# Performance work log

Hardware: AMD Instinct MI355X
Metric: run time of the kernel (lower is better)

Reference implementation:

```python
import jax, jax.numpy as jnp
import numpy as np

B, S, D, H, HD, FF, W = 2, 4096, 2048, 16, 128, 8192, 256
EPS = 1e-6
ROPE_BASE = 10000.0


def rmsnorm(x, w):
    return x * jax.lax.rsqrt(jnp.mean(x * x, axis=-1, keepdims=True) + EPS) * w


def apply_rope(x):
    # x: [B, H, S, hd]
    hd = x.shape[-1]
    inv = 1.0 / (ROPE_BASE ** (jnp.arange(0, hd, 2, dtype=jnp.float32) / hd))
    ang = jnp.arange(x.shape[2], dtype=jnp.float32)[:, None] * inv[None, :]  # [S, hd/2]
    cos, sin = jnp.cos(ang), jnp.sin(ang)
    x1, x2 = jnp.split(x, 2, axis=-1)
    return jnp.concatenate([x1 * cos - x2 * sin, x1 * sin + x2 * cos], axis=-1)


def setup_inputs() -> dict:
    key = jax.random.key(0)
    ks = jax.random.split(key, 12)
    sc = 0.02
    return {
        "x": jax.random.normal(ks[0], (B, S, D), jnp.float32),
        "Wq": jax.random.normal(ks[1], (D, D), jnp.float32) * sc,
        "Wk": jax.random.normal(ks[2], (D, D), jnp.float32) * sc,
        "Wv": jax.random.normal(ks[3], (D, D), jnp.float32) * sc,
        "Wo": jax.random.normal(ks[4], (D, D), jnp.float32) * sc,
        "qn_w": jnp.ones((HD,), jnp.float32),
        "kn_w": jnp.ones((HD,), jnp.float32),
        "sink_logit": jax.random.normal(ks[5], (H,), jnp.float32) * sc,
        "attn_norm_w": jnp.ones((D,), jnp.float32),
        "ffn_norm_w": jnp.ones((D,), jnp.float32),
        "Wg": jax.random.normal(ks[6], (D, FF), jnp.float32) * sc,
        "Wu": jax.random.normal(ks[7], (D, FF), jnp.float32) * sc,
        "Wd": jax.random.normal(ks[8], (FF, D), jnp.float32) * sc,
    }


def reference(x, Wq, Wk, Wv, Wo, qn_w, kn_w, sink_logit, attn_norm_w, ffn_norm_w, Wg, Wu, Wd):
    # ---- sliding-window attention sublayer ----
    h = rmsnorm(x, attn_norm_w)
    q = (h @ Wq).reshape(B, S, H, HD)
    k = (h @ Wk).reshape(B, S, H, HD)
    v = (h @ Wv).reshape(B, S, H, HD)
    q = rmsnorm(q, qn_w)
    k = rmsnorm(k, kn_w)
    q = apply_rope(q.transpose(0, 2, 1, 3))  # [B,H,S,hd]
    k = apply_rope(k.transpose(0, 2, 1, 3))
    v = v.transpose(0, 2, 1, 3)

    nb = S // W
    qb = q.reshape(B, H, nb, W, HD)
    kb = k.reshape(B, H, nb, W, HD)
    vb = v.reshape(B, H, nb, W, HD)
    # each query block attends to previous block + own block (window=W causal)
    kprev = jnp.concatenate([jnp.zeros_like(kb[:, :, :1]), kb[:, :, :-1]], axis=2)
    vprev = jnp.concatenate([jnp.zeros_like(vb[:, :, :1]), vb[:, :, :-1]], axis=2)
    kl = jnp.concatenate([kprev, kb], axis=3)  # [B,H,nb,2W,hd]
    vl = jnp.concatenate([vprev, vb], axis=3)

    qi = jnp.arange(W)
    kj = jnp.arange(2 * W)
    rel = W + qi[:, None] - kj[None, :]  # q_pos - kv_pos within block pair
    base = (rel >= 0) & (rel < W)  # causal + in-window, [W, 2W]
    blk = jnp.arange(nb)
    kv_pos_valid = (blk[:, None, None] * W - W + kj[None, None, :]) >= 0  # [nb,1,2W]
    mask = base[None, :, :] & kv_pos_valid  # [nb, W, 2W]

    scale = 1.0 / jnp.sqrt(jnp.float32(HD))
    scores = jnp.einsum("bhnqd,bhnkd->bhnqk", qb, kl) * scale
    scores = jnp.where(mask[None, None], scores, jnp.float32(-1e30))
    # attention sink: virtual kv slot 0 with per-head logit, zero value
    sink = jnp.broadcast_to(sink_logit.reshape(1, H, 1, 1, 1), scores.shape[:-1] + (1,))
    logits = jnp.concatenate([sink, scores], axis=-1)
    p = jax.nn.softmax(logits, axis=-1)
    out = jnp.einsum("bhnqk,bhnkd->bhnqd", p[..., 1:], vl)  # sink contributes 0
    out = out.reshape(B, H, S, HD).transpose(0, 2, 1, 3).reshape(B, S, D)
    x = x + out @ Wo

    # ---- SwiGLU FFN sublayer ----
    h2 = rmsnorm(x, ffn_norm_w)
    x = x + (jax.nn.silu(h2 @ Wg) * (h2 @ Wu)) @ Wd
    return x
```

## Files before the change

### kernel.cpp

```cpp
#include <hip/hip_runtime.h>
#include <hip/hip_bf16.h>
#include <stdint.h>

typedef __bf16 bf16_t;
typedef __bf16 bf16x8 __attribute__((ext_vector_type(8)));
typedef float f32x4 __attribute__((ext_vector_type(4)));

#define B_ 2
#define S_ 4096
#define D_ 2048
#define H_ 16
#define HD_ 128
#define FF_ 8192
#define W_ 256
#define NB_ 16
#define ROWS_ 8192
#define QS_ 6144

#define BAR() asm volatile("s_barrier" ::: "memory")

__device__ __forceinline__ bool det_bf16(const uint32_t* det) {
  return (det[0] & 0xFFFFu) == 0x3F80u;
}
__device__ __forceinline__ float ldS(const void* p, size_t i, bool isbf) {
  return isbf ? (float)((const bf16_t*)p)[i] : ((const float*)p)[i];
}
__device__ __forceinline__ void ld8(const void* p, size_t i, bool isbf,
                                    float* f) {
  if (isbf) {
    bf16x8 v = *(const bf16x8*)((const bf16_t*)p + i);
#pragma unroll
    for (int j = 0; j < 8; ++j) f[j] = (float)v[j];
  } else {
    const float* s = (const float*)p + i;
    float4 a = *(const float4*)s;
    float4 b = *(const float4*)(s + 4);
    f[0] = a.x; f[1] = a.y; f[2] = a.z; f[3] = a.w;
    f[4] = b.x; f[5] = b.y; f[6] = b.z; f[7] = b.w;
  }
}

__device__ __forceinline__ void gld_lds16(const bf16_t* g, bf16_t* l) {
  __builtin_amdgcn_global_load_lds(
      (const __attribute__((address_space(1))) uint32_t*)g,
      (__attribute__((address_space(3))) uint32_t*)l, 16, 0, 0);
}

__global__ __launch_bounds__(256)
void transpose_k(const void* __restrict__ src, bf16_t* __restrict__ dst,
                 int R, int C, const uint32_t* __restrict__ det) {
  __shared__ __align__(16) bf16_t tile[64][72];
  const bool isbf = det_bf16(det);
  const int nbc = C >> 6;
  const int br = blockIdx.x / nbc, bc = blockIdx.x % nbc;
  const int t = threadIdx.x;
#pragma unroll
  for (int rnd = 0; rnd < 2; ++rnd) {
    int chunk = t + rnd * 256;
    int r = chunk >> 3;
    int c8 = (chunk & 7) << 3;
    float f[8];
    ld8(src, (size_t)(br * 64 + r) * C + bc * 64 + c8, isbf, f);
    union { bf16_t e[8]; int4 v; } u;
#pragma unroll
    for (int j = 0; j < 8; ++j) u.e[j] = (bf16_t)f[j];
    *(int4*)&tile[r][c8] = u.v;
  }
  __syncthreads();
#pragma unroll
  for (int rnd = 0; rnd < 2; ++rnd) {
    int chunk = t + rnd * 256;
    int cc = chunk >> 3;
    int r8 = (chunk & 7) << 3;
    union { bf16_t e[8]; int4 v; } u;
#pragma unroll
    for (int j = 0; j < 8; ++j) u.e[j] = tile[r8 + j][cc];
    *(int4*)&dst[(size_t)(bc * 64 + cc) * R + br * 64 + r8] = u.v;
  }
}

__global__ __launch_bounds__(256)
void rmsnorm_in_k(const void* __restrict__ x, const void* __restrict__ w,
                  bf16_t* __restrict__ out, const uint32_t* __restrict__ det) {
  __shared__ float sm[4];
  const bool isbf = det_bf16(det);
  const size_t row = blockIdx.x;
  const int i0 = threadIdx.x << 3;
  float f[8], ss = 0.f;
  ld8(x, row * D_ + i0, isbf, f);
#pragma unroll
  for (int j = 0; j < 8; ++j) ss += f[j] * f[j];
#pragma unroll
  for (int off = 1; off < 64; off <<= 1) ss += __shfl_xor(ss, off, 64);
  if ((threadIdx.x & 63) == 0) sm[threadIdx.x >> 6] = ss;
  __syncthreads();
  float tot = sm[0] + sm[1] + sm[2] + sm[3];
  float rs = rsqrtf(tot * (1.0f / D_) + 1e-6f);
  float wf[8];
  ld8(w, i0, isbf, wf);
  bf16x8 res;
#pragma unroll
  for (int j = 0; j < 8; ++j) res[j] = (bf16_t)(f[j] * rs * wf[j]);
  *(bf16x8*)&out[row * D_ + i0] = res;
}

__global__ __launch_bounds__(256)
void rmsnorm_f32_k(const float* __restrict__ x, const void* __restrict__ w,
                   bf16_t* __restrict__ out, const uint32_t* __restrict__ det) {
  __shared__ float sm[4];
  const bool isbf = det_bf16(det);
  const size_t row = blockIdx.x;
  const int i0 = threadIdx.x << 3;
  float4 a = *(const float4*)&x[row * D_ + i0];
  float4 b = *(const float4*)&x[row * D_ + i0 + 4];
  float f[8] = {a.x, a.y, a.z, a.w, b.x, b.y, b.z, b.w};
  float ss = 0.f;
#pragma unroll
  for (int j = 0; j < 8; ++j) ss += f[j] * f[j];
#pragma unroll
  for (int off = 1; off < 64; off <<= 1) ss += __shfl_xor(ss, off, 64);
  if ((threadIdx.x & 63) == 0) sm[threadIdx.x >> 6] = ss;
  __syncthreads();
  float tot = sm[0] + sm[1] + sm[2] + sm[3];
  float rs = rsqrtf(tot * (1.0f / D_) + 1e-6f);
  float wf[8];
  ld8(w, i0, isbf, wf);
  bf16x8 res;
#pragma unroll
  for (int j = 0; j < 8; ++j) res[j] = (bf16_t)(f[j] * rs * wf[j]);
  *(bf16x8*)&out[row * D_ + i0] = res;
}

__global__ __launch_bounds__(256)
void qknorm_rope_k(bf16_t* __restrict__ qkv, const void* __restrict__ qw,
                   const void* __restrict__ kw,
                   const uint32_t* __restrict__ det) {
  const bool isbf = det_bf16(det);
  const int wv = threadIdx.x >> 6;
  const int i = threadIdx.x & 63;
  const int idx = blockIdx.x * 4 + wv;
  const int row = idx >> 4;
  const int s = row & (S_ - 1);
  const int h = idx & 15;
  bf16_t* qp = qkv + (size_t)row * QS_ + h * HD_;
  bf16_t* kp = qp + 2048;

  float inv = exp2f((float)i * -0.20762050593046014f);
  float ang = (float)s * inv;
  float sn, cs;
  sincosf(ang, &sn, &cs);

#pragma unroll
  for (int t = 0; t < 2; ++t) {
    bf16_t* p = (t == 0) ? qp : kp;
    const void* w = (t == 0) ? qw : kw;
    float x1 = (float)p[i], x2 = (float)p[i + 64];
    float ss = x1 * x1 + x2 * x2;
#pragma unroll
    for (int off = 1; off < 64; off <<= 1) ss += __shfl_xor(ss, off, 64);
    float rs = rsqrtf(ss * (1.0f / HD_) + 1e-6f);
    float n1 = x1 * rs * ldS(w, i, isbf);
    float n2 = x2 * rs * ldS(w, i + 64, isbf);
    p[i] = (bf16_t)(n1 * cs - n2 * sn);
    p[i + 64] = (bf16_t)(n1 * sn + n2 * cs);
  }
}

#define TQ 8192

template <int EPI>
__global__ __launch_bounds__(512, 2)
void gemm256_k(const bf16_t* __restrict__ A, const bf16_t* __restrict__ Bt,
               void* __restrict__ C, const void* __restrict__ aux,
               const uint32_t* __restrict__ det, int M, int N, int K) {
  extern __shared__ __align__(16) bf16_t lds[];
  bf16_t* Ab = lds;
  bf16_t* Bb = lds + 2 * TQ;

  bool isbf = false;
  if constexpr (EPI == 1 || EPI == 3) isbf = det_bf16(det);

  const int tid = threadIdx.x;
  const int lane = tid & 63, wid = tid >> 6;
  const int l15 = lane & 15, l4 = lane >> 4;
  const int wm = wid >> 2, wn = wid & 3;

  const int nwg = gridDim.x;
  const int nbn = N >> 8;
  const int orig = blockIdx.x;
  const int q8 = nwg >> 3, r8 = nwg & 7, xcd = orig & 7;
  const int swz = (xcd < r8 ? xcd * (q8 + 1) : r8 * (q8 + 1) + (xcd - r8) * q8)
                + (orig >> 3);
  const int grp = swz / (4 * nbn);
  const int rem = swz % (4 * nbn);
  const int bm = grp * 4 + (rem & 3);
  const int bn = rem >> 2;

  const bf16_t* Ag = A + (size_t)(bm * 256) * K;
  const bf16_t* Bg = Bt + (size_t)(bn * 256) * K;

  const int c0 = tid, c1 = 512 + tid;
  const int r0 = c0 >> 2, r1 = c1 >> 2;
  const size_t goff0 = (size_t)r0 * K + (((c0 & 3) ^ ((r0 >> 1) & 3)) << 3);
  const size_t goff1 = (size_t)r1 * K + (((c1 & 3) ^ ((r1 >> 1) & 3)) << 3);
  const int loff0 = c0 * 8, loff1 = c1 * 8;

  auto stage = [&](int tt) {
    bf16_t* la = Ab + (tt & 1) * TQ;
    bf16_t* lb = Bb + (tt & 1) * TQ;
    const size_t k0 = (size_t)tt << 5;
    gld_lds16(Ag + k0 + goff0, la + loff0);
    gld_lds16(Ag + k0 + goff1, la + loff1);
    gld_lds16(Bg + k0 + goff0, lb + loff0);
    gld_lds16(Bg + k0 + goff1, lb + loff1);
  };

  int aoff[8], boff[4];
#pragma unroll
  for (int m = 0; m < 8; ++m) {
    int R = wm * 128 + m * 16 + l15;
    aoff[m] = R * 32 + ((l4 ^ ((R >> 1) & 3)) << 3);
  }
#pragma unroll
  for (int n = 0; n < 4; ++n) {
    int R = wn * 64 + n * 16 + l15;
    boff[n] = R * 32 + ((l4 ^ ((R >> 1) & 3)) << 3);
  }

  f32x4 acc[8][4] = {};
  const int nt = K >> 5;

  stage(0);
  asm volatile("s_waitcnt vmcnt(0)" ::: "memory");
  BAR();

  for (int t = 0; t < nt; ++t) {
    const bf16_t* a = Ab + (t & 1) * TQ;
    const bf16_t* b = Bb + (t & 1) * TQ;

    if (t + 1 < nt) stage(t + 1);

    bf16x8 af[8], bfr[4];
#pragma unroll
    for (int n = 0; n < 4; ++n) bfr[n] = *(const bf16x8*)&b[boff[n]];
#pragma unroll
    for (int m = 0; m < 8; ++m) af[m] = *(const bf16x8*)&a[aoff[m]];

#pragma unroll
    for (int m = 0; m < 8; ++m)
#pragma unroll
      for (int n = 0; n < 4; ++n)
        acc[m][n] = __builtin_amdgcn_mfma_f32_16x16x32_bf16(af[m], bfr[n],
                                                            acc[m][n], 0, 0, 0);

    asm volatile("s_waitcnt vmcnt(0)" ::: "memory");
    BAR();
  }

#pragma unroll
  for (int m8 = 0; m8 < 8; ++m8) {
#pragma unroll
    for (int r = 0; r < 4; ++r) {
      const int row = bm * 256 + wm * 128 + m8 * 16 + l4 * 4 + r;
#pragma unroll
      for (int n = 0; n < 4; ++n) {
        const int col = bn * 256 + wn * 64 + n * 16 + l15;
        const size_t idx = (size_t)row * N + col;
        const float val = acc[m8][n][r];
        if constexpr (EPI == 0) {
          ((bf16_t*)C)[idx] = (bf16_t)val;
        } else if constexpr (EPI == 1) {
          ((float*)C)[idx] = ldS(aux, idx, isbf) + val;
        } else if constexpr (EPI == 2) {
          float g = (float)((const bf16_t*)aux)[idx];
          float sg = g / (1.f + __expf(-g));
          ((bf16_t*)C)[idx] = (bf16_t)(sg * val);
        } else {
          float v = ((const float*)aux)[idx] + val;
          if (isbf) ((bf16_t*)C)[idx] = (bf16_t)v;
          else      ((float*)C)[idx] = v;
        }
      }
    }
  }
}

__global__ __launch_bounds__(512)
void attn_k(const bf16_t* __restrict__ QKV, const void* __restrict__ sink,
            bf16_t* __restrict__ O, const uint32_t* __restrict__ det) {
  __shared__ __align__(16) bf16_t Ks[64][128];
  __shared__ __align__(16) bf16_t Vt[128][64];
  __shared__ __align__(16) bf16_t Ps[8][32][64];

  const bool isbf = det_bf16(det);
  const int bx = blockIdx.x;
  const int n = bx & (NB_ - 1);
  const int h = (bx >> 4) & (H_ - 1);
  const int b = bx >> 8;
  const int tid = threadIdx.x;
  const int wv = tid >> 6, lane = tid & 63;
  const int l15 = lane & 15, l4 = lane >> 4;
  const size_t qkvbase = (size_t)b * S_ * QS_ + h * HD_;
  const size_t obase = ((size_t)b * S_ * H_ + h) * HD_;
  const int q0 = n * W_;
  const int wq = wv * 32;

  bf16x8 qf[2][4];
#pragma unroll
  for (int mi = 0; mi < 2; ++mi)
#pragma unroll
    for (int kb = 0; kb < 4; ++kb) {
      int s = q0 + wq + mi * 16 + l15;
      qf[mi][kb] = *(const bf16x8*)&QKV[qkvbase + (size_t)s * QS_ + kb * 32 + l4 * 8];
    }

  const float sinkl = ldS(sink, h, isbf);
  float m_run[2][4], l_run[2][4];
#pragma unroll
  for (int mi = 0; mi < 2; ++mi)
#pragma unroll
    for (int r = 0; r < 4; ++r) { m_run[mi][r] = sinkl; l_run[mi][r] = 1.0f; }
  f32x4 oacc[2][8] = {};

  const int kvbase = q0 - W_;
  const float scale = 0.088388347648318447f;

  for (int c = 0; c < 8; ++c) {
    __syncthreads();
#pragma unroll
    for (int rnd = 0; rnd < 2; ++rnd) {
      int chunk = tid + rnd * 512;
      int r = chunk >> 4;
      int c8 = (chunk & 15) << 3;
      int sk = kvbase + c * 64 + r;
      int4 kv = {0, 0, 0, 0}, vvv = {0, 0, 0, 0};
      if (sk >= 0) {
        const bf16_t* src = &QKV[qkvbase + (size_t)sk * QS_ + c8];
        kv = *(const int4*)(src + 2048);
        vvv = *(const int4*)(src + 4096);
      }
      *(int4*)&Ks[r][c8] = kv;
      const bf16_t* pv = (const bf16_t*)&vvv;
#pragma unroll
      for (int j = 0; j < 8; ++j) Vt[c8 + j][r] = pv[j];
    }
    __syncthreads();

    bool any = (c * 64 + 63 >= wq + 1) && (c * 64 <= wq + 31 + W_);
    if (n == 0 && c < 4) any = false;
    if (!any) continue;

    f32x4 sacc[2][4] = {};
#pragma unroll
    for (int kb = 0; kb < 4; ++kb) {
      bf16x8 kf[4];
#pragma unroll
      for (int ni = 0; ni < 4; ++ni)
        kf[ni] = *(const bf16x8*)&Ks[ni * 16 + l15][kb * 32 + l4 * 8];
#pragma unroll
      for (int mi = 0; mi < 2; ++mi)
#pragma unroll
        for (int ni = 0; ni < 4; ++ni)
          sacc[mi][ni] = __builtin_amdgcn_mfma_f32_16x16x32_bf16(
              qf[mi][kb], kf[ni], sacc[mi][ni], 0, 0, 0);
    }

#pragma unroll
    for (int mi = 0; mi < 2; ++mi) {
#pragma unroll
      for (int r = 0; r < 4; ++r) {
        const int qi = wq + mi * 16 + l4 * 4 + r;
        float mx = -3.0e38f;
#pragma unroll
        for (int ni = 0; ni < 4; ++ni) {
          int kj = c * 64 + ni * 16 + l15;
          bool ok = (kj > qi) && (kj <= qi + W_) && (n > 0 || kj >= W_);
          float sv = ok ? sacc[mi][ni][r] * scale : -1.0e30f;
          sacc[mi][ni][r] = sv;
          mx = fmaxf(mx, sv);
        }
#pragma unroll
        for (int off = 1; off < 16; off <<= 1)
          mx = fmaxf(mx, __shfl_xor(mx, off, 64));
        float mo = m_run[mi][r];
        float mn = fmaxf(mo, mx);
        float alpha = __expf(mo - mn);
        m_run[mi][r] = mn;
        float rs = 0.f;
#pragma unroll
        for (int ni = 0; ni < 4; ++ni) {
          float p = __expf(sacc[mi][ni][r] - mn);
          sacc[mi][ni][r] = p;
          rs += p;
        }
#pragma unroll
        for (int off = 1; off < 16; off <<= 1) rs += __shfl_xor(rs, off, 64);
        l_run[mi][r] = l_run[mi][r] * alpha + rs;
#pragma unroll
        for (int ni = 0; ni < 8; ++ni) oacc[mi][ni][r] *= alpha;
      }
    }

#pragma unroll
    for (int mi = 0; mi < 2; ++mi)
#pragma unroll
      for (int ni = 0; ni < 4; ++ni)
#pragma unroll
        for (int r = 0; r < 4; ++r)
          Ps[wv][mi * 16 + l4 * 4 + r][ni * 16 + l15] = (bf16_t)sacc[mi][ni][r];

#pragma unroll
    for (int kb2 = 0; kb2 < 2; ++kb2) {
      bf16x8 pf[2];
#pragma unroll
      for (int mi = 0; mi < 2; ++mi)
        pf[mi] = *(const bf16x8*)&Ps[wv][mi * 16 + l15][kb2 * 32 + l4 * 8];
#pragma unroll
      for (int ni = 0; ni < 8; ++ni) {
        bf16x8 vf = *(const bf16x8*)&Vt[ni * 16 + l15][kb2 * 32 + l4 * 8];
#pragma unroll
        for (int mi = 0; mi < 2; ++mi)
          oacc[mi][ni] = __builtin_amdgcn_mfma_f32_16x16x32_bf16(
              pf[mi], vf, oacc[mi][ni], 0, 0, 0);
      }
    }
  }

#pragma unroll
  for (int mi = 0; mi < 2; ++mi)
#pragma unroll
    for (int r = 0; r < 4; ++r) {
      float inv = 1.0f / l_run[mi][r];
      int s = q0 + wq + mi * 16 + l4 * 4 + r;
#pragma unroll
      for (int ni = 0; ni < 8; ++ni)
        O[obase + (size_t)s * (H_ * HD_) + ni * 16 + l15] =
            (bf16_t)(oacc[mi][ni][r] * inv);
    }
}

extern "C" void kernel_launch(void* const* d_in, const int* in_sizes, int n_in,
                              void* d_out, int out_size, void* d_ws,
                              size_t ws_size, hipStream_t stream) {
  const void* x   = d_in[0];
  const void* Wq  = d_in[1];
  const void* Wk  = d_in[2];
  const void* Wv  = d_in[3];
  const void* Wo  = d_in[4];
  const void* qnw = d_in[5];
  const void* knw = d_in[6];
  const void* snk = d_in[7];
  const void* anw = d_in[8];
  const void* fnw = d_in[9];
  const void* Wg  = d_in[10];
  const void* Wu  = d_in[11];
  const void* Wd  = d_in[12];
  const uint32_t* det = (const uint32_t*)anw;

  char* ws = (char*)d_ws;
  const size_t MB = 1024ull * 1024ull;
  bf16_t* WT  = (bf16_t*)(ws + 0 * MB);
  bf16_t* hb  = (bf16_t*)(ws + 32 * MB);
  bf16_t* qkv = (bf16_t*)(ws + 64 * MB);
  bf16_t* ao  = (bf16_t*)(ws + 160 * MB);
  float* xm   = (float*)(ws + 192 * MB);
  bf16_t* gb  = (bf16_t*)(ws + 64 * MB);

  const int LDSZ = 65536;
  hipFuncSetAttribute((const void*)gemm256_k<0>,
                      hipFuncAttributeMaxDynamicSharedMemorySize, LDSZ);
  hipFuncSetAttribute((const void*)gemm256_k<1>,
                      hipFuncAttributeMaxDynamicSharedMemorySize, LDSZ);
  hipFuncSetAttribute((const void*)gemm256_k<2>,
                      hipFuncAttributeMaxDynamicSharedMemorySize, LDSZ);
  hipFuncSetAttribute((const void*)gemm256_k<3>,
                      hipFuncAttributeMaxDynamicSharedMemorySize, LDSZ);

  rmsnorm_in_k<<<ROWS_, 256, 0, stream>>>(x, anw, hb, det);

  transpose_k<<<32 * 32, 256, 0, stream>>>(Wq, WT, 2048, 2048, det);
  transpose_k<<<32 * 32, 256, 0, stream>>>(Wk, WT + 2048 * 2048, 2048, 2048, det);
  transpose_k<<<32 * 32, 256, 0, stream>>>(Wv, WT + 2 * 2048 * 2048, 2048, 2048, det);
  gemm256_k<0><<<32 * 24, 512, LDSZ, stream>>>(hb, WT, qkv, nullptr, det,
                                               8192, 6144, 2048);

  qknorm_rope_k<<<B_ * S_ * H_ / 4, 256, 0, stream>>>(qkv, qnw, knw, det);

  attn_k<<<B_ * H_ * NB_, 512, 0, stream>>>(qkv, snk, ao, det);

  transpose_k<<<32 * 32, 256, 0, stream>>>(Wo, WT, 2048, 2048, det);
  gemm256_k<1><<<32 * 8, 512, LDSZ, stream>>>(ao, WT, xm, x, det, 8192, 2048, 2048);

  rmsnorm_f32_k<<<ROWS_, 256, 0, stream>>>(xm, fnw, hb, det);

  transpose_k<<<32 * 128, 256, 0, stream>>>(Wg, WT, 2048, 8192, det);
  gemm256_k<0><<<32 * 32, 512, LDSZ, stream>>>(hb, WT, gb, nullptr, det, 8192, 8192, 2048);
  transpose_k<<<32 * 128, 256, 0, stream>>>(Wu, WT, 2048, 8192, det);
  gemm256_k<2><<<32 * 32, 512, LDSZ, stream>>>(hb, WT, gb, gb, det, 8192, 8192, 2048);
  transpose_k<<<128 * 32, 256, 0, stream>>>(Wd, WT, 8192, 2048, det);
  gemm256_k<3><<<32 * 8, 512, LDSZ, stream>>>(gb, WT, d_out, xm, det, 8192, 2048, 8192);

  (void)in_sizes; (void)n_in; (void)out_size; (void)ws_size;
}
```

Baseline: 1.360 ms.

## Restructure GEMM main loop into 64-wide K tiles with staged quarter-tile prefetch

Doubles the K tile of the 256x256 bf16 GEMM from 32 to 64 and splits each tile into four quarter MFMA phases. Global-to-LDS loads for the next tiles are interleaved between phases, with partial vmcnt waits and s_setprio around the MFMA bursts, so memory traffic overlaps compute instead of being drained by a full wait each iteration. The LDS swizzle changes to an 8-way XOR for 64-element rows. The cost is 128 KB of LDS per block, which limits occupancy to one block per CU despite launch_bounds(512,2), plus many more barriers.

```diff
diff --git a/kernel.cpp b/kernel.cpp
--- a/kernel.cpp
+++ b/kernel.cpp
@@ -18,6 +18,7 @@
 #define QS_ 6144
 
 #define BAR() asm volatile("s_barrier" ::: "memory")
+#define LGKM0() asm volatile("s_waitcnt lgkmcnt(0)" ::: "memory")
 
 __device__ __forceinline__ bool det_bf16(const uint32_t* det) {
   return (det[0] & 0xFFFFu) == 0x3F80u;
@@ -166,7 +167,7 @@
   }
 }
 
-#define TQ 8192
+#define TQ 16384
 
 template <int EPI>
 __global__ __launch_bounds__(512, 2)
@@ -174,8 +175,10 @@
                void* __restrict__ C, const void* __restrict__ aux,
                const uint32_t* __restrict__ det, int M, int N, int K) {
   extern __shared__ __align__(16) bf16_t lds[];
-  bf16_t* Ab = lds;
-  bf16_t* Bb = lds + 2 * TQ;
+  bf16_t* A0 = lds;
+  bf16_t* A1 = lds + TQ;
+  bf16_t* B0 = lds + 2 * TQ;
+  bf16_t* B1 = lds + 3 * TQ;
 
   bool isbf = false;
   if constexpr (EPI == 1 || EPI == 3) isbf = det_bf16(det);
@@ -199,61 +202,92 @@
   const bf16_t* Ag = A + (size_t)(bm * 256) * K;
   const bf16_t* Bg = Bt + (size_t)(bn * 256) * K;
 
-  const int c0 = tid, c1 = 512 + tid;
-  const int r0 = c0 >> 2, r1 = c1 >> 2;
-  const size_t goff0 = (size_t)r0 * K + (((c0 & 3) ^ ((r0 >> 1) & 3)) << 3);
-  const size_t goff1 = (size_t)r1 * K + (((c1 & 3) ^ ((r1 >> 1) & 3)) << 3);
-  const int loff0 = c0 * 8, loff1 = c1 * 8;
-
-  auto stage = [&](int tt) {
-    bf16_t* la = Ab + (tt & 1) * TQ;
-    bf16_t* lb = Bb + (tt & 1) * TQ;
-    const size_t k0 = (size_t)tt << 5;
-    gld_lds16(Ag + k0 + goff0, la + loff0);
-    gld_lds16(Ag + k0 + goff1, la + loff1);
-    gld_lds16(Bg + k0 + goff0, lb + loff0);
-    gld_lds16(Bg + k0 + goff1, lb + loff1);
+  const int st_r = tid >> 3, st_u = tid & 7;
+  auto stq = [&](const bf16_t* g, int q, int kt, bf16_t* lb) {
+    int row = q * 64 + st_r;
+    int col = (kt << 6) + ((st_u ^ (row & 7)) << 3);
+    gld_lds16(g + (size_t)row * K + col, lb + row * 64 + st_u * 8);
   };
 
-  int aoff[8], boff[4];
-#pragma unroll
-  for (int m = 0; m < 8; ++m) {
-    int R = wm * 128 + m * 16 + l15;
-    aoff[m] = R * 32 + ((l4 ^ ((R >> 1) & 3)) << 3);
-  }
-#pragma unroll
-  for (int n = 0; n < 4; ++n) {
-    int R = wn * 64 + n * 16 + l15;
-    boff[n] = R * 32 + ((l4 ^ ((R >> 1) & 3)) << 3);
-  }
+  bf16x8 af[4][2], bf0[2][2], bf1[2][2];
+  auto rdA = [&](const bf16_t* a, int qm) {
+#pragma unroll
+    for (int m = 0; m < 4; ++m)
+#pragma unroll
+      for (int ks = 0; ks < 2; ++ks) {
+        int R = wm * 128 + qm * 64 + m * 16 + l15;
+        af[m][ks] = *(const bf16x8*)&a[R * 64 + ((((ks << 2) | l4) ^ (R & 7)) << 3)];
+      }
+  };
+  auto rdB = [&](const bf16_t* b, int qn, bf16x8 (*bfr)[2]) {
+#pragma unroll
+    for (int n = 0; n < 2; ++n)
+#pragma unroll
+      for (int ks = 0; ks < 2; ++ks) {
+        int R = wn * 64 + qn * 32 + n * 16 + l15;
+        bfr[n][ks] = *(const bf16x8*)&b[R * 64 + ((((ks << 2) | l4) ^ (R & 7)) << 3)];
+      }
+  };
 
   f32x4 acc[8][4] = {};
-  const int nt = K >> 5;
-
-  stage(0);
-  asm volatile("s_waitcnt vmcnt(0)" ::: "memory");
+  auto mma = [&](bf16x8 (*bfr)[2], int qm, int qn) {
+    __builtin_amdgcn_s_setprio(1);
+#pragma unroll
+    for (int m = 0; m < 4; ++m)
+#pragma unroll
+      for (int n = 0; n < 2; ++n)
+#pragma unroll
+        for (int ks = 0; ks < 2; ++ks)
+          acc[qm * 4 + m][qn * 2 + n] = __builtin_amdgcn_mfma_f32_16x16x32_bf16(
+              af[m][ks], bfr[n][ks], acc[qm * 4 + m][qn * 2 + n], 0, 0, 0);
+    __builtin_amdgcn_s_setprio(0);
+  };
+
+  const int nt = K >> 6;
+  const int ni = nt >> 1;
+
+#pragma unroll
+  for (int q = 0; q < 4; ++q) stq(Ag, q, 0, A0);
+#pragma unroll
+  for (int q = 0; q < 4; ++q) stq(Bg, q, 0, B0);
+  stq(Ag, 0, 1, A1); stq(Ag, 2, 1, A1);
+#pragma unroll
+  for (int q = 0; q < 4; ++q) stq(Bg, q, 1, B1);
+  asm volatile("s_waitcnt vmcnt(6)" ::: "memory");
   BAR();
 
-  for (int t = 0; t < nt; ++t) {
-    const bf16_t* a = Ab + (t & 1) * TQ;
-    const bf16_t* b = Bb + (t & 1) * TQ;
-
-    if (t + 1 < nt) stage(t + 1);
-
-    bf16x8 af[8], bfr[4];
-#pragma unroll
-    for (int n = 0; n < 4; ++n) bfr[n] = *(const bf16x8*)&b[boff[n]];
-#pragma unroll
-    for (int m = 0; m < 8; ++m) af[m] = *(const bf16x8*)&a[aoff[m]];
-
-#pragma unroll
-    for (int m = 0; m < 8; ++m)
-#pragma unroll
-      for (int n = 0; n < 4; ++n)
-        acc[m][n] = __builtin_amdgcn_mfma_f32_16x16x32_bf16(af[m], bfr[n],
-                                                            acc[m][n], 0, 0, 0);
-
-    asm volatile("s_waitcnt vmcnt(0)" ::: "memory");
+  for (int it = 0; it < ni; ++it) {
+    const int t0 = 2 * it, t1 = 2 * it + 1;
+    const bool pf = (it + 1 < ni);
+
+    rdA(A0, 0); rdB(B0, 0, bf0);
+    stq(Ag, 1, t1, A1); stq(Ag, 3, t1, A1);
+    BAR(); LGKM0(); mma(bf0, 0, 0); BAR();
+    rdB(B0, 1, bf1);
+    if (pf) { stq(Ag, 0, t0 + 2, A0); stq(Ag, 2, t0 + 2, A0); }
+    BAR(); LGKM0(); mma(bf1, 0, 1); BAR();
+    rdA(A0, 1);
+    if (pf) { stq(Bg, 0, t0 + 2, B0); stq(Bg, 1, t0 + 2, B0); }
+    BAR(); LGKM0(); mma(bf0, 1, 0); BAR();
+    if (pf) { stq(Bg, 2, t0 + 2, B0); stq(Bg, 3, t0 + 2, B0); }
+    BAR(); LGKM0(); mma(bf1, 1, 1);
+    if (pf) { asm volatile("s_waitcnt vmcnt(6)" ::: "memory"); }
+    else    { asm volatile("s_waitcnt vmcnt(0)" ::: "memory"); }
+    BAR();
+
+    rdA(A1, 0); rdB(B1, 0, bf0);
+    if (pf) { stq(Ag, 1, t0 + 2, A0); stq(Ag, 3, t0 + 2, A0); }
+    BAR(); LGKM0(); mma(bf0, 0, 0); BAR();
+    rdB(B1, 1, bf1);
+    if (pf) { stq(Ag, 0, t1 + 2, A1); stq(Ag, 2, t1 + 2, A1); }
+    BAR(); LGKM0(); mma(bf1, 0, 1); BAR();
+    rdA(A1, 1);
+    if (pf) { stq(Bg, 0, t1 + 2, B1); stq(Bg, 1, t1 + 2, B1); }
+    BAR(); LGKM0(); mma(bf0, 1, 0); BAR();
+    if (pf) { stq(Bg, 2, t1 + 2, B1); stq(Bg, 3, t1 + 2, B1); }
+    BAR(); LGKM0(); mma(bf1, 1, 1);
+    if (pf) { asm volatile("s_waitcnt vmcnt(6)" ::: "memory"); }
+    else    { asm volatile("s_waitcnt vmcnt(0)" ::: "memory"); }
     BAR();
   }
 
@@ -466,7 +500,7 @@
   float* xm   = (float*)(ws + 192 * MB);
   bf16_t* gb  = (bf16_t*)(ws + 64 * MB);
 
-  const int LDSZ = 65536;
+  const int LDSZ = 131072;
   hipFuncSetAttribute((const void*)gemm256_k<0>,
                       hipFuncAttributeMaxDynamicSharedMemorySize, LDSZ);
   hipFuncSetAttribute((const void*)gemm256_k<1>,
```

Measured after the change: 1.317 ms. -3.2%, faster.
